# Optimization experiments

Hardware: AMD Instinct MI355X
Metric: run time of the kernel (lower is better)

The kernel has to match this reference:

```python
import jax, jax.numpy as jnp
import numpy as np

RUNS, WAYS, SHOT, QUERIES, D = 512, 5, 5, 15, 640
NS, QS = WAYS * SHOT, WAYS * QUERIES
LAM, ALPHA, UPDATE_RATE, EPOCHS = 10.0, 0.7, 0.6, 3
OT_EPS, OT_MAXITERS = 1e-3, 1000


def compute_entropy(P):
    # P: (runs, n, ways); normalized entropy per row
    P = P + 1e-12
    P = P / P.sum(axis=2, keepdims=True)
    H = -jnp.sum(P * jnp.log(P), axis=2)
    return H / jnp.log(jnp.asarray(P.shape[2], P.dtype))


def sq_cdist(a, b):
    # squared euclidean distance, (runs,n,d) x (runs,m,d) -> (runs,n,m)
    d2 = (a * a).sum(-1)[:, :, None] + (b * b).sum(-1)[:, None, :] \
         - 2.0 * jnp.einsum('bnd,bmd->bnm', a, b)
    return jnp.maximum(d2, 0.0)


def get_distance(f1, f2):
    return jnp.exp(-LAM * sq_cdist(f1, f2))


def build_graph(W):
    n = W.shape[1]
    W = W * (1.0 - jnp.eye(n, dtype=W.dtype)[None])  # zero diagonal
    Dm = W.sum(-1) ** -0.5                            # D^{-1/2}
    return Dm[:, None, :] * W * Dm[:, :, None]


def sinkhorn(M, n_l, labels, eps):
    # faithful port of compute_optimal_transport (class_balance=True)
    nr, n, ways = M.shape
    r = jnp.ones((nr, n), M.dtype)
    c = jnp.full((nr, ways), float(n // ways), M.dtype)  # ones*n//ways (floor)
    onehot = jax.nn.one_hot(labels[:, :n_l], ways, dtype=M.dtype) if n_l > 0 else None

    def cond(st):
        P, u, it = st
        return (jnp.max(jnp.abs(u - P.sum(2))) > eps) & (it <= OT_MAXITERS)

    def body(st):
        P, u, it = st
        u = P.sum(2)
        P = P * (r / u)[:, :, None]
        P = P * (c / P.sum(1))[:, None, :]
        if n_l > 0:
            P = P.at[:, :n_l, :].set(onehot)  # fill_(0) + scatter_(2, labels, 1)
        return P, u, it + 1

    P, _, _ = jax.lax.while_loop(cond, body, (M, jnp.zeros((nr, n), M.dtype), jnp.int32(1)))
    return P


def get_prob(features, proto, ys):
    d2 = sq_cdist(features, proto)
    Pq = jnp.exp(-LAM * d2[:, NS:])
    Pq = sinkhorn(Pq, 0, ys, 1e-3)
    Ps = jax.nn.one_hot(ys, WAYS, dtype=d2.dtype)  # scatter on support rows
    return jnp.concatenate([Ps, Pq], axis=1)


def _forward(xs, xq, ys, yq):
    features = jnp.concatenate([xs, xq], axis=1)           # (runs, ns+qs, d)
    labels = jnp.concatenate([ys, yq], axis=1)
    runs = features.shape[0]
    proto = features[:, :NS].reshape(runs, WAYS, SHOT, -1).mean(axis=2)
    Z = None
    for _ in range(EPOCHS):  # (pre-loop Z / Inverse_W in torch code are dead code)
        features = features[:, :NS + QS]
        Z = get_prob(features, proto, ys)
        ent = compute_entropy(Z)
        Z = Z * (1.0 - ent[..., None])
        # update_prototype
        new_proto = jnp.einsum('bnk,bnd->bkd', Z, features) / Z.sum(axis=1)[..., None]
        proto = (1.0 - UPDATE_RATE) * proto + UPDATE_RATE * new_proto
        dist_proto = get_distance(proto, proto)
        score = compute_entropy(dist_proto)
        omega = ent.mean(axis=1, keepdims=True)
        mask = (score < omega).astype(Z.dtype)             # (runs, ways)
        add_proto = proto * mask[..., None]
        dist_proto = dist_proto * mask[..., None]
        features = jnp.concatenate([features, add_proto], axis=1)  # (runs, ns+qs+ways, d)
        Z = jnp.concatenate([Z, dist_proto], axis=1)
        dist = get_distance(features, features)
        W = build_graph(dist)
        n = features.shape[1]
        Inv = jnp.linalg.inv(jnp.eye(n, dtype=W.dtype)[None] - ALPHA * W)
        Z = Inv @ Z                                         # (I - aW)^{-1} diffusion
        Z = sinkhorn(Z, NS, ys, OT_EPS)
    olabels = jnp.argmax(Z[:, :NS + QS], axis=2)
    matches = (labels == olabels).astype(jnp.float32)
    return matches[:, NS:].mean(axis=1)                     # acc_test: (runs,)


def setup_inputs() -> dict:
    key = jax.random.key(0)
    k1, k2, k3 = jax.random.split(key, 3)
    scale = 0.04  # keeps exp(-lam*dist^2) in fp32 normal range
    xs = scale * jax.random.normal(k1, (RUNS, NS, D), dtype=jnp.float32)
    xq = scale * jax.random.normal(k2, (RUNS, QS, D), dtype=jnp.float32)
    # support labels must be class-block ordered (proto reshape assumes it)
    ys = jnp.tile(jnp.repeat(jnp.arange(WAYS, dtype=jnp.int32), SHOT)[None, :], (RUNS, 1))
    yq = jax.random.randint(k3, (RUNS, QS), 0, WAYS, dtype=jnp.int32)
    return {'xs': xs, 'xq': xq, 'ys': ys, 'yq': yq}


def reference(xs, xq, ys, yq):
    return _forward(xs, xq, ys, yq)
```

## Files before the change

kernel.cpp:

```cpp
#include <hip/hip_runtime.h>
#include <math.h>

#define RUNS  512
#define WAYS  5
#define SHOT  5
#define NSUP  25
#define NQ    75
#define N0    100
#define NF    105
#define DIM   640
#define LAMB  10.0f
#define ALF   0.7f
#define UPD   0.6f
#define OT_EPSF 0.001f
#define OT_MAXIT 1000

#define NTILE 14
#define FCH_ROWS 112
#define FCH_STRIDE 36
#define HALF 56
#define CHUNK 64

#define W_WAKE(g)  ((g) * 16)
#define W_C1(g)    (1024 + (g) * 16)
#define W_C2(s)    (2048 + (s) * 16)
#define W_C0       2176
#define W_SLOT(b,g) (2304 + ((b) * 16 + (g)) * 16)

struct __align__(16) Smem {
  float fch[FCH_ROWS * FCH_STRIDE];
  float pbuf[WAYS * DIM];
  float rowk[112];
  float colk[112];
  float Zm[NF * WAYS];
  float ent[NF];
  float fnorm[112];
  float dm[112];
  float rsumh[112];
  float dp[WAYS * WAYS];
  float pn[WAYS];
  float maskv[WAYS];
  float red[4];
  float snap[16][44];
  float pivotv;
  int foundsh;
  int ysl[NSUP];
};
static_assert(sizeof(Smem) <= 40 * 1024, "LDS: 2 blocks/CU (80KB of 160KB)");

__device__ __forceinline__ float wsum(float v) {
#pragma unroll
  for (int o = 32; o > 0; o >>= 1) v += __shfl_xor(v, o, 64);
  return v;
}
__device__ __forceinline__ float bsum(float v, float* red, int tid) {
  v = wsum(v);
  __syncthreads();
  if ((tid & 63) == 0) red[tid >> 6] = v;
  __syncthreads();
  return (red[0] + red[1]) + (red[2] + red[3]);
}

template <int CTRL>
__device__ __forceinline__ float dppx(float v) {
  union U { float f; int i; } a, b;
  a.f = v;
  b.i = __builtin_amdgcn_update_dpp(0, a.i, CTRL, 0xF, 0xF, true);
  return b.f;
}
__device__ __forceinline__ float rsum16(float v) {
  v += dppx<0xB1>(v);
  v += dppx<0x4E>(v);
  v += dppx<0x141>(v);
  v += dppx<0x140>(v);
  return v;
}
__device__ __forceinline__ float rmax16(float v) {
  v = fmaxf(v, dppx<0xB1>(v));
  v = fmaxf(v, dppx<0x4E>(v));
  v = fmaxf(v, dppx<0x141>(v));
  v = fmaxf(v, dppx<0x140>(v));
  return v;
}

__device__ __forceinline__ void gbar_found(Smem& sm, unsigned* ctl, unsigned& bi,
                                           int tid, int r, int buf, int base) {
  __syncthreads();
  if (tid == 0) {
    const unsigned tgt = 8u * bi + 7u;
    const unsigned seq = bi + 1u;
    int found = -1;
    bool isroot = false;
    unsigned a = __hip_atomic_fetch_add(&ctl[W_C1(r >> 3)], 1u,
                                        __ATOMIC_RELEASE, __HIP_MEMORY_SCOPE_AGENT);
    if (a == tgt) {
      unsigned b = __hip_atomic_fetch_add(&ctl[W_C2(r >> 6)], 1u,
                                          __ATOMIC_RELEASE, __HIP_MEMORY_SCOPE_AGENT);
      if (b == tgt) {
        unsigned c = __hip_atomic_fetch_add(&ctl[W_C0], 1u,
                                            __ATOMIC_RELEASE, __HIP_MEMORY_SCOPE_AGENT);
        if (c == tgt) isroot = true;
      }
    }
    if (isroot) {
      unsigned long long m = 0ull;
#pragma unroll
      for (int g = 0; g < 16; g++)
        m |= __hip_atomic_load((unsigned long long*)(ctl + W_SLOT(buf, g)),
                               __ATOMIC_RELAXED, __HIP_MEMORY_SCOPE_AGENT);
      for (int p = 0; p < CHUNK; p++) {
        int k = base + p + 1;
        bool cond = (((m >> p) & 1ull) != 0ull) && (k <= OT_MAXIT);
        if (!cond) { found = p; break; }
      }
#pragma unroll
      for (int g = 0; g < 16; g++)
        __hip_atomic_store((unsigned long long*)(ctl + W_SLOT(buf, g)), 0ull,
                           __ATOMIC_RELAXED, __HIP_MEMORY_SCOPE_AGENT);
      unsigned pk = seq | ((unsigned)(found + 1) << 16);
      __hip_atomic_store(&ctl[W_WAKE(0)], pk, __ATOMIC_RELEASE, __HIP_MEMORY_SCOPE_AGENT);
#pragma unroll 4
      for (int g = 1; g < 64; g++)
        __hip_atomic_store(&ctl[W_WAKE(g)], pk, __ATOMIC_RELAXED, __HIP_MEMORY_SCOPE_AGENT);
    } else {
      unsigned w;
      for (;;) {
        w = __hip_atomic_load(&ctl[W_WAKE(r >> 3)], __ATOMIC_RELAXED, __HIP_MEMORY_SCOPE_AGENT);
        if ((w & 0xffffu) >= seq) break;
        __builtin_amdgcn_s_sleep(8);
      }
      found = (int)((w >> 16) & 0xffu) - 1;
    }
    sm.foundsh = found;
    bi++;
  }
  __syncthreads();
}

__device__ __forceinline__ float entropy5(const float* z) {
  float p[5]; float t = 0.f;
#pragma unroll
  for (int w = 0; w < 5; w++) { p[w] = z[w] + 1e-12f; t += p[w]; }
  float H = 0.f;
#pragma unroll
  for (int w = 0; w < 5; w++) { float q = p[w] / t; H -= q * logf(q); }
  return H / logf(5.0f);
}

__device__ __forceinline__ float loadF(const float* xs, const float* xq, int r, int i, int d) {
  return (i < NSUP) ? xs[(r * NSUP + i) * DIM + d] : xq[(r * NQ + (i - NSUP)) * DIM + d];
}

template <int S, bool CLAMP>
__device__ void sinkhorn_dpp(Smem& sm, unsigned* ctl, unsigned& bi, int rowOff,
                             int n, float cval, int tid, int r, int& sidx) {
  const int lane = tid & 63;
  const int wv = tid >> 6;
  const int l16 = lane & 15;
  const bool grp0 = lane < 16;
  float p[S][5], u[S];
  int yv[S];
  bool val[S];
  if (wv == 0) {
#pragma unroll
    for (int k = 0; k < S; k++) {
      int rr = 16 * k + l16;
      val[k] = rr < n;
#pragma unroll
      for (int w = 0; w < 5; w++)
        p[k][w] = val[k] ? sm.Zm[(rowOff + rr) * 5 + w] : 0.f;
      u[k] = 0.f;
      yv[k] = (CLAMP && rr < NSUP) ? sm.ysl[rr < NSUP ? rr : 0] : -1;
    }
  }

  auto body = [&]() -> float {
    float res = 0.f;
#pragma unroll
    for (int k = 0; k < S; k++) {
      float t = p[k][0];
#pragma unroll
      for (int w = 1; w < 5; w++) t += p[k][w];
      res = fmaxf(res, val[k] ? fabsf(u[k] - t) : 0.f);
      u[k] = t;
      float i0 = val[k] ? 1.0f / t : 0.f;
#pragma unroll
      for (int w = 0; w < 5; w++) p[k][w] *= i0;
    }
    res = rmax16(res);
#pragma unroll
    for (int w = 0; w < 5; w++) {
      float cs = p[0][w];
#pragma unroll
      for (int k = 1; k < S; k++) cs += p[k][w];
      cs = rsum16(cs);
      float f = cval / cs;
#pragma unroll
      for (int k = 0; k < S; k++) p[k][w] *= f;
    }
    if (CLAMP) {
#pragma unroll
      for (int k = 0; k < S; k++) {
        if (16 * k < NSUP) {
          if (yv[k] >= 0) {
#pragma unroll
            for (int w = 0; w < 5; w++) p[k][w] = (yv[k] == w) ? 1.0f : 0.0f;
          }
        }
      }
    }
    return res;
  };

  int base = 0;
  while (true) {
    unsigned long long mask = 0ull;
    if (wv == 0) {
      if (grp0) {
#pragma unroll
        for (int k = 0; k < S; k++) {
#pragma unroll
          for (int w = 0; w < 5; w++) sm.snap[l16][k * 5 + w] = p[k][w];
          sm.snap[l16][35 + k] = u[k];
        }
      }
#pragma unroll 1
      for (int pp = 0; pp < CHUNK; pp++) {
        float res = body();
        if (res > OT_EPSF) mask |= (1ull << pp);
      }
      if (lane == 0)
        __hip_atomic_fetch_or((unsigned long long*)(ctl + W_SLOT(sidx & 1, r >> 5)), mask,
                              __ATOMIC_RELAXED, __HIP_MEMORY_SCOPE_AGENT);
    }
    gbar_found(sm, ctl, bi, tid, r, sidx & 1, base);
    int found = sm.foundsh;
    sidx++;
    if (found >= 0) {
      if (wv == 0) {
#pragma unroll
        for (int k = 0; k < S; k++) {
#pragma unroll
          for (int w = 0; w < 5; w++) p[k][w] = sm.snap[l16][k * 5 + w];
          u[k] = sm.snap[l16][35 + k];
        }
#pragma unroll 1
        for (int pp = 0; pp < found; pp++) (void)body();
        if (grp0) {
#pragma unroll
          for (int k = 0; k < S; k++) {
            if (val[k]) {
              int rr = 16 * k + l16;
#pragma unroll
              for (int w = 0; w < 5; w++)
                sm.Zm[(rowOff + rr) * 5 + w] = p[k][w];
            }
          }
        }
      }
      __syncthreads();
      return;
    }
    base += CHUNK;
  }
}

__global__ void init_kernel(unsigned* __restrict__ ctl, float* __restrict__ out) {
  int i = blockIdx.x * blockDim.x + threadIdx.x;
  if (i < 4096) __hip_atomic_store(&ctl[i], 0u, __ATOMIC_RELAXED, __HIP_MEMORY_SCOPE_AGENT);
  if (i < RUNS) out[i] = -1.0f;
}

__global__ __launch_bounds__(256, 2) void fsl_kernel(
    const float* __restrict__ xs, const float* __restrict__ xq,
    const int* __restrict__ ys, const int* __restrict__ yq,
    float* __restrict__ out, unsigned* __restrict__ ctl) {
  __shared__ Smem sm;
  const int tid = threadIdx.x;
  const int r = blockIdx.x;
  const int lane = tid & 63, wid = tid >> 6;
  unsigned bi = 0;
  int sidx = 0;

  for (int i = wid; i < N0; i += 4) {
    float p = 0.f;
    for (int d = lane; d < DIM; d += 64) { float v = loadF(xs, xq, r, i, d); p += v * v; }
    p = wsum(p);
    if (lane == 0) sm.fnorm[i] = p;
  }
  if (tid < NSUP) sm.ysl[tid] = ys[r * NSUP + tid];
  for (int idx = tid; idx < WAYS * DIM; idx += 256) {
    int w = idx / DIM, d = idx % DIM;
    float sacc = 0.f;
#pragma unroll
    for (int s5 = 0; s5 < SHOT; s5++) sacc += xs[(r * NSUP + w * SHOT + s5) * DIM + d];
    sm.pbuf[idx] = sacc / 5.0f;
  }
  __syncthreads();

  int ti = 0, tj = 0;
  if (tid < 210) {
    int t = tid >> 1;
    while (t >= NTILE - ti) { t -= NTILE - ti; ti++; }
    tj = ti + t;
  }
  const int hcol = tid & 1;
  const bool own = tid < 210;
  const int erow = own ? (tid % 105) : 0;
  const int hh = own ? (tid / 105) : 0;
  const int jbase = HALF * hh;

  float (*band)[112] = (float (*)[112])sm.fch;

  for (int ep = 0; ep < 3; ep++) {
    for (int w = wid; w < WAYS; w += 4) {
      float p = 0.f;
      for (int d = lane; d < DIM; d += 64) { float v = sm.pbuf[w * DIM + d]; p += v * v; }
      p = wsum(p);
      if (lane == 0) sm.pn[w] = p;
    }
    __syncthreads();
    for (int pq = wid; pq < NQ * WAYS; pq += 4) {
      int q = pq / 5, w = pq % 5;
      float dt = 0.f;
      for (int d = lane; d < DIM; d += 64)
        dt += xq[(r * NQ + q) * DIM + d] * sm.pbuf[w * DIM + d];
      dt = wsum(dt);
      if (lane == 0) {
        float d2 = fmaxf(sm.fnorm[NSUP + q] + sm.pn[w] - 2.0f * dt, 0.0f);
        sm.Zm[(NSUP + q) * 5 + w] = expf(-LAMB * d2);
      }
    }
    __syncthreads();
    sinkhorn_dpp<5, false>(sm, ctl, bi, NSUP, NQ, 15.0f, tid, r, sidx);
    if (tid < NSUP * 5) { int i = tid / 5, w = tid % 5; sm.Zm[i * 5 + w] = (sm.ysl[i] == w) ? 1.0f : 0.0f; }
    __syncthreads();
    if (tid < N0) {
      float e = entropy5(&sm.Zm[tid * 5]);
      sm.ent[tid] = e;
      float f1 = 1.0f - e;
#pragma unroll
      for (int w = 0; w < 5; w++) sm.Zm[tid * 5 + w] *= f1;
    }
    __syncthreads();
    float zs[5];
#pragma unroll
    for (int w = 0; w < 5; w++) zs[w] = bsum(tid < N0 ? sm.Zm[tid * 5 + w] : 0.f, sm.red, tid);
    for (int d = tid; d < DIM; d += 256) {
      float a[5] = {0.f, 0.f, 0.f, 0.f, 0.f};
      for (int i = 0; i < N0; i++) {
        float v = loadF(xs, xq, r, i, d);
#pragma unroll
        for (int w = 0; w < 5; w++) a[w] += sm.Zm[i * 5 + w] * v;
      }
#pragma unroll
      for (int w = 0; w < 5; w++) {
        float old = sm.pbuf[w * DIM + d];
        sm.pbuf[w * DIM + d] = (1.0f - UPD) * old + UPD * (a[w] / zs[w]);
      }
    }
    __syncthreads();
    for (int w = wid; w < WAYS; w += 4) {
      float p = 0.f;
      for (int d = lane; d < DIM; d += 64) { float v = sm.pbuf[w * DIM + d]; p += v * v; }
      p = wsum(p);
      if (lane == 0) sm.pn[w] = p;
    }
    __syncthreads();
    for (int pp5 = wid; pp5 < 25; pp5 += 4) {
      int a5 = pp5 / 5, b5 = pp5 % 5;
      float dt = 0.f;
      for (int d = lane; d < DIM; d += 64)
        dt += sm.pbuf[a5 * DIM + d] * sm.pbuf[b5 * DIM + d];
      dt = wsum(dt);
      if (lane == 0) {
        float d2 = fmaxf(sm.pn[a5] + sm.pn[b5] - 2.0f * dt, 0.0f);
        sm.dp[pp5] = expf(-LAMB * d2);
      }
    }
    __syncthreads();
    float omega = bsum(tid < N0 ? sm.ent[tid] : 0.f, sm.red, tid) / 100.0f;
    if (tid < WAYS) {
      float sc = entropy5(&sm.dp[tid * 5]);
      sm.maskv[tid] = (sc < omega) ? 1.0f : 0.0f;
    }
    __syncthreads();
    if (tid < WAYS) sm.fnorm[N0 + tid] = sm.maskv[tid] * sm.pn[tid];
    if (tid < 25) { int a5 = tid / 5, b5 = tid % 5; sm.Zm[(N0 + a5) * 5 + b5] = sm.dp[tid] * sm.maskv[a5]; }
    __syncthreads();
    float acc[32];
#pragma unroll
    for (int z = 0; z < 32; z++) acc[z] = 0.f;
    for (int c = 0; c < 20; c++) {
      for (int idx = tid; idx < FCH_ROWS * 32; idx += 256) {
        int i = idx >> 5, dc = idx & 31;
        float v = 0.f;
        int d = c * 32 + dc;
        if (i < N0) v = loadF(xs, xq, r, i, d);
        else if (i < NF) v = sm.maskv[i - N0] * sm.pbuf[(i - N0) * DIM + d];
        int gg = dc >> 2, rm = dc & 3;
        sm.fch[i * FCH_STRIDE + (((gg ^ ((i >> 3) & 7)) << 2) | rm)] = v;
      }
      __syncthreads();
      if (tid < 210) {
        int i0 = ti * 8, j0 = tj * 8 + 4 * hcol, si = ti & 7, sj = tj & 7;
#pragma unroll
        for (int g = 0; g < 8; g++) {
          float4 a4[8], b4[4];
#pragma unroll
          for (int rr = 0; rr < 8; rr++)
            a4[rr] = *(const float4*)&sm.fch[(i0 + rr) * FCH_STRIDE + ((g ^ si) << 2)];
#pragma unroll
          for (int cc = 0; cc < 4; cc++)
            b4[cc] = *(const float4*)&sm.fch[(j0 + cc) * FCH_STRIDE + ((g ^ sj) << 2)];
#pragma unroll
          for (int rr = 0; rr < 8; rr++)
#pragma unroll
            for (int cc = 0; cc < 4; cc++)
              acc[rr * 4 + cc] += a4[rr].x * b4[cc].x + a4[rr].y * b4[cc].y +
                                  a4[rr].z * b4[cc].z + a4[rr].w * b4[cc].w;
        }
      }
      __syncthreads();
    }
    float Areg[HALF];
    float rsum = 0.f;
    for (int b = 0; b < NTILE; b++) {
      if (tid < 210) {
        if (ti == b) {
#pragma unroll
          for (int rr = 0; rr < 8; rr++)
#pragma unroll
            for (int cc = 0; cc < 4; cc++)
              band[rr][8 * tj + 4 * hcol + cc] = acc[rr * 4 + cc];
        }
        if (tj == b && ti != b) {
#pragma unroll
          for (int rr = 0; rr < 8; rr++)
#pragma unroll
            for (int cc = 0; cc < 4; cc++)
              band[4 * hcol + cc][8 * ti + rr] = acc[rr * 4 + cc];
        }
      }
      __syncthreads();
      if (own && (erow >> 3) == b) {
        int lr = erow & 7;
#pragma unroll
        for (int jj = 0; jj < HALF; jj++) {
          int j = jbase + jj;
          float wv = 0.f;
          if (j < NF && j != erow) {
            float d2 = fmaxf(sm.fnorm[erow] + sm.fnorm[j] - 2.0f * band[lr][j], 0.0f);
            wv = expf(-LAMB * d2);
          }
          Areg[jj] = wv;
          rsum += wv;
        }
      }
      __syncthreads();
    }
    if (own && hh == 1) sm.rsumh[erow] = rsum;
    __syncthreads();
    if (own && hh == 0) sm.dm[erow] = 1.0f / sqrtf(rsum + sm.rsumh[erow]);
    __syncthreads();
    float cnext = 0.f;
    if (own) {
      float dme = sm.dm[erow];
#pragma unroll
      for (int jj = 0; jj < HALF; jj++) {
        int j = jbase + jj;
        float t = (j < NF) ? (sm.dm[j] * Areg[jj]) * dme : 0.f;
        Areg[jj] = ((j == erow) ? 1.0f : 0.0f) - ALF * t;
      }
      if (hh == 0) cnext = Areg[0];
    }
    if (tid < 112) sm.rowk[tid] = 0.f;
    __syncthreads();
    for (int k = 0; k < NF; k++) {
      int hk = (k < HALF) ? 0 : 1;
      if (own && hh == hk) {
        if (erow == k) { sm.pivotv = cnext; sm.colk[k] = 0.f; }
        else sm.colk[erow] = cnext;
      }
      __syncthreads();
      float pinv = 1.0f / sm.pivotv;
      if (own && erow == k) {
#pragma unroll
        for (int jj = 0; jj < HALF; jj++) {
          int j = jbase + jj;
          if (j > k && j < NF) { Areg[jj] *= pinv; sm.rowk[j] = Areg[jj]; }
        }
        if (hh == hk) sm.rowk[k] = 0.f;
        if (hh == 0) {
#pragma unroll
          for (int w = 0; w < 5; w++) sm.Zm[k * 5 + w] *= pinv;
        }
      }
      __syncthreads();
      if (own) {
        float m = sm.colk[erow];
#pragma unroll
        for (int jj = 0; jj < HALF; jj += 4) {
          float4 rk = *(const float4*)&sm.rowk[jbase + jj];
          Areg[jj + 0] -= m * rk.x;
          Areg[jj + 1] -= m * rk.y;
          Areg[jj + 2] -= m * rk.z;
          Areg[jj + 3] -= m * rk.w;
        }
#pragma unroll
        for (int jj = 0; jj < HALF; jj++)
          if (jbase + jj == k + 1) cnext = Areg[jj];
        if (hh == 0 && erow != k) {
#pragma unroll
          for (int w = 0; w < 5; w++) sm.Zm[erow * 5 + w] -= m * sm.Zm[k * 5 + w];
        }
      }
      __syncthreads();
    }
    sinkhorn_dpp<7, true>(sm, ctl, bi, 0, NF, 21.0f, tid, r, sidx);
  }

  float mt = 0.f;
  if (tid < NQ) {
    int row = NSUP + tid;
    float best = sm.Zm[row * 5]; int bl = 0;
#pragma unroll
    for (int w = 1; w < 5; w++) { float v = sm.Zm[row * 5 + w]; if (v > best) { best = v; bl = w; } }
    mt = (yq[r * NQ + tid] == bl) ? 1.0f : 0.0f;
  }
  float tot = bsum(mt, sm.red, tid);
  if (tid == 0) out[r] = tot / 75.0f;
}

extern "C" void kernel_launch(void* const* d_in, const int* in_sizes, int n_in,
                              void* d_out, int out_size, void* d_ws, size_t ws_size,
                              hipStream_t stream) {
  const float* xs = (const float*)d_in[0];
  const float* xq = (const float*)d_in[1];
  const int* ys = (const int*)d_in[2];
  const int* yq = (const int*)d_in[3];
  float* out = (float*)d_out;
  unsigned* ctl = (unsigned*)d_ws;
  init_kernel<<<dim3(16), dim3(256), 0, stream>>>(ctl, out);
  fsl_kernel<<<dim3(RUNS), dim3(256), 0, stream>>>(xs, xq, ys, yq, out, ctl);
}
```

Measured before the change: 6.864 ms.

## Run full Sinkhorn iteration budget speculatively per grid barrier with multiple snapshots

Each grid-wide barrier round now runs up to 1024 Sinkhorn iterations in 64-iteration subchunks instead of one 64-iteration chunk. The per-subchunk convergence masks go into a larger atomic slot array, and LDS snapshots are taken every 128 iterations. After the barrier, each block restores the nearest snapshot and replays the remaining iterations up to the stopping point. This is meant to remove most grid barrier rounds, at the cost of wasted speculative iterations past convergence and more LDS, which may reduce occupancy.

```diff
diff --git a/kernel.cpp b/kernel.cpp
--- a/kernel.cpp
+++ b/kernel.cpp
@@ -19,13 +19,17 @@
 #define FCH_ROWS 112
 #define FCH_STRIDE 36
 #define HALF 56
-#define CHUNK 64
+
+#define CHUNK 1024
+#define SUBCH 64
+#define NSUB  16
+#define NSNAP 8
 
 #define W_WAKE(g)  ((g) * 16)
-#define W_C1(g)    (1024 + (g) * 16)
-#define W_C2(s)    (2048 + (s) * 16)
-#define W_C0       2176
-#define W_SLOT(b,g) (2304 + ((b) * 16 + (g)) * 16)
+#define W_C1(g)    (1024 + (g))
+#define W_C2(s)    (1088 + (s) * 16)
+#define W_C0       1216
+#define W_SLOTW(b,g) (1232 + ((b) * 16 + (g)) * 32)
 
 struct __align__(16) Smem {
   float fch[FCH_ROWS * FCH_STRIDE];
@@ -41,12 +45,12 @@
   float pn[WAYS];
   float maskv[WAYS];
   float red[4];
-  float snap[16][44];
+  float snap[NSNAP][16][44];
   float pivotv;
   int foundsh;
   int ysl[NSUP];
 };
-static_assert(sizeof(Smem) <= 40 * 1024, "LDS: 2 blocks/CU (80KB of 160KB)");
+static_assert(sizeof(Smem) <= 64 * 1024, "LDS: 2 blocks/CU (113 of 160 KB)");
 
 __device__ __forceinline__ float wsum(float v) {
 #pragma unroll
@@ -103,20 +107,25 @@
       }
     }
     if (isroot) {
-      unsigned long long m = 0ull;
-#pragma unroll
+#pragma unroll 1
+      for (int w2 = 0; w2 < NSUB && found < 0; w2++) {
+        unsigned long long m = 0ull;
+#pragma unroll
+        for (int g = 0; g < 16; g++)
+          m |= __hip_atomic_load((unsigned long long*)(ctl + W_SLOTW(buf, g)) + w2,
+                                 __ATOMIC_RELAXED, __HIP_MEMORY_SCOPE_AGENT);
+        for (int p2 = 0; p2 < SUBCH; p2++) {
+          int k = base + w2 * SUBCH + p2 + 1;
+          bool cond = (((m >> p2) & 1ull) != 0ull) && (k <= OT_MAXIT);
+          if (!cond) { found = w2 * SUBCH + p2; break; }
+        }
+      }
+#pragma unroll 1
       for (int g = 0; g < 16; g++)
-        m |= __hip_atomic_load((unsigned long long*)(ctl + W_SLOT(buf, g)),
-                               __ATOMIC_RELAXED, __HIP_MEMORY_SCOPE_AGENT);
-      for (int p = 0; p < CHUNK; p++) {
-        int k = base + p + 1;
-        bool cond = (((m >> p) & 1ull) != 0ull) && (k <= OT_MAXIT);
-        if (!cond) { found = p; break; }
-      }
-#pragma unroll
-      for (int g = 0; g < 16; g++)
-        __hip_atomic_store((unsigned long long*)(ctl + W_SLOT(buf, g)), 0ull,
-                           __ATOMIC_RELAXED, __HIP_MEMORY_SCOPE_AGENT);
+#pragma unroll
+        for (int w2 = 0; w2 < NSUB; w2++)
+          __hip_atomic_store((unsigned long long*)(ctl + W_SLOTW(buf, g)) + w2, 0ull,
+                             __ATOMIC_RELAXED, __HIP_MEMORY_SCOPE_AGENT);
       unsigned pk = seq | ((unsigned)(found + 1) << 16);
       __hip_atomic_store(&ctl[W_WAKE(0)], pk, __ATOMIC_RELEASE, __HIP_MEMORY_SCOPE_AGENT);
 #pragma unroll 4
@@ -129,7 +138,7 @@
         if ((w & 0xffffu) >= seq) break;
         __builtin_amdgcn_s_sleep(8);
       }
-      found = (int)((w >> 16) & 0xffu) - 1;
+      found = (int)(w >> 16) - 1;
     }
     sm.foundsh = found;
     bi++;
@@ -214,38 +223,43 @@
 
   int base = 0;
   while (true) {
-    unsigned long long mask = 0ull;
     if (wv == 0) {
-      if (grp0) {
-#pragma unroll
-        for (int k = 0; k < S; k++) {
-#pragma unroll
-          for (int w = 0; w < 5; w++) sm.snap[l16][k * 5 + w] = p[k][w];
-          sm.snap[l16][35 + k] = u[k];
-        }
-      }
 #pragma unroll 1
-      for (int pp = 0; pp < CHUNK; pp++) {
-        float res = body();
-        if (res > OT_EPSF) mask |= (1ull << pp);
-      }
-      if (lane == 0)
-        __hip_atomic_fetch_or((unsigned long long*)(ctl + W_SLOT(sidx & 1, r >> 5)), mask,
-                              __ATOMIC_RELAXED, __HIP_MEMORY_SCOPE_AGENT);
+      for (int sc = 0; sc < NSUB; sc++) {
+        if ((sc & 1) == 0 && grp0) {
+          int si = sc >> 1;
+#pragma unroll
+          for (int k = 0; k < S; k++) {
+#pragma unroll
+            for (int w = 0; w < 5; w++) sm.snap[si][l16][k * 5 + w] = p[k][w];
+            sm.snap[si][l16][35 + k] = u[k];
+          }
+        }
+        unsigned long long mw = 0ull;
+#pragma unroll 1
+        for (int pp = 0; pp < SUBCH; pp++) {
+          float res = body();
+          if (res > OT_EPSF) mw |= (1ull << pp);
+        }
+        if (lane == 0)
+          __hip_atomic_fetch_or((unsigned long long*)(ctl + W_SLOTW(sidx & 1, r >> 5)) + sc,
+                                mw, __ATOMIC_RELAXED, __HIP_MEMORY_SCOPE_AGENT);
+      }
     }
     gbar_found(sm, ctl, bi, tid, r, sidx & 1, base);
     int found = sm.foundsh;
     sidx++;
     if (found >= 0) {
       if (wv == 0) {
+        int si = found >> 7, rep = found & 127;
 #pragma unroll
         for (int k = 0; k < S; k++) {
 #pragma unroll
-          for (int w = 0; w < 5; w++) p[k][w] = sm.snap[l16][k * 5 + w];
-          u[k] = sm.snap[l16][35 + k];
+          for (int w = 0; w < 5; w++) p[k][w] = sm.snap[si][l16][k * 5 + w];
+          u[k] = sm.snap[si][l16][35 + k];
         }
 #pragma unroll 1
-        for (int pp = 0; pp < found; pp++) (void)body();
+        for (int pp = 0; pp < rep; pp++) (void)body();
         if (grp0) {
 #pragma unroll
           for (int k = 0; k < S; k++) {
```

Result: slower. 10.07 ms (+46.7%).
